# Optimization experiments

Measured on AMD Instinct MI355X. Metric: run time of the kernel, lower is better.

## Reference

```python
import jax, jax.numpy as jnp
import numpy as np

# Index conventions from the original repo's stop net
STOP_NET_STOP_IX = 0
STOP_NET_CONTINUE_IX = 1

T = 65536   # trajectory length
B = 64      # number of options (b)
A = 32      # number of low-level actions (a)


def setup_inputs() -> dict:
    key = jax.random.key(0)
    k1, k2, k3, k4 = jax.random.split(key, 4)
    # Normalized log-probabilities, as produced by abstract_policy_net
    action_logps = jax.nn.log_softmax(jax.random.normal(k1, (T + 1, B, A), jnp.float32), axis=-1)
    stop_logps = jax.nn.log_softmax(jax.random.normal(k2, (T + 1, B, 2), jnp.float32), axis=-1)
    start_logps = jax.nn.log_softmax(jax.random.normal(k3, (T + 1, B), jnp.float32), axis=-1)
    actions = jax.random.randint(k4, (T,), 0, A)
    return {
        "action_logps": action_logps,
        "stop_logps": stop_logps,
        "start_logps": start_logps,
        "actions": actions,
    }


def _hmm_neg_logp(action_logps, stop_logps, start_logps, actions):
    Tlen = actions.shape[0]
    b = start_logps.shape[1]
    # chosen-action log-probs per timestep: (T, b) = action_logps[i, :, actions[i]]
    ac = jnp.take_along_axis(action_logps[:Tlen], actions[:, None, None], axis=2)[..., 0]
    f0 = start_logps[0] + ac[0]                      # (b,)
    eye = jnp.eye(b, dtype=bool)

    def step(f_prev, xs):
        stop_i, start_i, ac_i = xs                   # (b,2), (b,), (b,)
        beta = stop_i[:, STOP_NET_STOP_IX]           # log p(stop)
        omb = stop_i[:, STOP_NET_CONTINUE_IX]        # log p(continue)
        # trans_fn[i,j] = logaddexp(beta_i + start_j, [i==j] * omb_i)
        m = beta[:, None] + start_i[None, :]         # (b, b)
        trans = jnp.where(eye, jnp.logaddexp(m, omb[:, None]), m)
        f = jax.nn.logsumexp(f_prev[:, None] + trans, axis=0) + ac_i
        return f, None

    xs = (stop_logps[1:Tlen], start_logps[1:Tlen], ac[1:Tlen])
    f, _ = jax.lax.scan(step, f0, xs)
    total_logp = jax.nn.logsumexp(f + stop_logps[Tlen, :, STOP_NET_STOP_IX])
    return -total_logp


def reference(action_logps, stop_logps, start_logps, actions):
    return _hmm_neg_logp(action_logps, stop_logps, start_logps, actions)
```

## Files before the change

kernel.cpp:

```cpp
#include <hip/hip_runtime.h>
#include <math.h>

#define T_LEN 65536
#define CHUNK 128
#define NCHUNK 512

#define CONS_BYTES ((size_t)T_LEN * 192 * 4)
#define BUFA_OFF   CONS_BYTES
#define BUFA_BYTES ((size_t)NCHUNK * 4096 * 4)
#define BUFB_OFF   (BUFA_OFF + BUFA_BYTES)
#define BUFB_BYTES ((size_t)(NCHUNK / 2) * 4096 * 4)
#define WS_NEEDED  (BUFB_OFF + BUFB_BYTES)

__global__ __launch_bounds__(256) void k_prep(const float* __restrict__ alp,
                                              const float* __restrict__ stp,
                                              const float* __restrict__ srt,
                                              const int* __restrict__ act,
                                              float* __restrict__ cons) {
    int gid = blockIdx.x * 256 + threadIdx.x;
    int t = gid >> 6;
    int b = gid & 63;
    if (t >= T_LEN) return;
    int a = act[t];
    float ac = __expf(alp[(size_t)t * 2048 + b * 32 + a]);
    float sp = __expf(srt[t * 64 + b]);
    float2 st2 = ((const float2*)stp)[t * 64 + b];
    float bp = __expf(st2.x);
    float cp = __expf(st2.y);
    size_t o = (size_t)t * 192 + b;
    cons[o]       = ac * sp;
    cons[o + 64]  = ac * cp;
    cons[o + 128] = bp;
}

#define K2_LOAD(BUF, II) do {                                                  \
    int ic_ = (II); if (ic_ > T_LEN - 1) ic_ = T_LEN - 1;                      \
    const float4* p_ = (const float4*)(cons + (size_t)ic_ * 192 + r0);         \
    const float4* q_ = (const float4*)(cons + (size_t)ic_ * 192 + 64 + r0);    \
    const float4* s_ = (const float4*)(cons + (size_t)ic_ * 192 + 128 + r0);   \
    _Pragma("unroll") for (int u = 0; u < 4; ++u) as##BUF[u] = p_[u];          \
    _Pragma("unroll") for (int u = 0; u < 4; ++u) aw##BUF[u] = q_[u];          \
    _Pragma("unroll") for (int u = 0; u < 4; ++u) bp##BUF[u] = s_[u];          \
} while (0)

#define K2_STEP(BUF, JJ) do {                                                  \
    const int i_ = ibase + (JJ);                                               \
    if (i_ < T_LEN) {                                                          \
        float sp_ = 0.f;                                                       \
        _Pragma("unroll")                                                      \
        for (int u = 0; u < 4; ++u) {                                          \
            sp_ += bp##BUF[u].x * m[4*u+0] + bp##BUF[u].y * m[4*u+1]           \
                 + bp##BUF[u].z * m[4*u+2] + bp##BUF[u].w * m[4*u+3];          \
        }                                                                      \
        part[g][col] = sp_;                                                    \
        __syncthreads();                                                       \
        float sig = part[0][col] + part[1][col] + part[2][col] + part[3][col]; \
        __syncthreads();                                                       \
        _Pragma("unroll")                                                      \
        for (int u = 0; u < 4; ++u) {                                          \
            m[4*u+0] = fmaf(aw##BUF[u].x, m[4*u+0], as##BUF[u].x * sig);       \
            m[4*u+1] = fmaf(aw##BUF[u].y, m[4*u+1], as##BUF[u].y * sig);       \
            m[4*u+2] = fmaf(aw##BUF[u].z, m[4*u+2], as##BUF[u].z * sig);       \
            m[4*u+3] = fmaf(aw##BUF[u].w, m[4*u+3], as##BUF[u].w * sig);       \
        }                                                                      \
        if (((JJ) & 3) == 3) {                                                 \
            float mxv = 0.f;                                                   \
            _Pragma("unroll")                                                  \
            for (int k = 0; k < 16; ++k) mxv = fmaxf(mxv, m[k]);               \
            part[g][col] = mxv;                                                \
            __syncthreads();                                                   \
            float cmax = fmaxf(fmaxf(part[0][col], part[1][col]),              \
                               fmaxf(part[2][col], part[3][col]));             \
            __syncthreads();                                                   \
            if (cmax > 0.f) {                                                  \
                float inv = 1.0f / cmax;                                       \
                _Pragma("unroll")                                              \
                for (int k = 0; k < 16; ++k) m[k] *= inv;                      \
                lsc += __logf(cmax);                                           \
            } else { lsc = -1e30f; }                                           \
        }                                                                      \
    }                                                                          \
} while (0)

__global__ __launch_bounds__(256) void k_chunk(const float* __restrict__ cons,
                                               float* __restrict__ mats) {
    const int tid = threadIdx.x;
    const int col = tid & 63;
    const int g = tid >> 6;
    const int r0 = __builtin_amdgcn_readfirstlane(g << 4);
    __shared__ float part[4][64];
    float m[16];
#pragma unroll
    for (int k = 0; k < 16; ++k) m[k] = (r0 + k == col) ? 1.0f : 0.0f;
    float lsc = 0.0f;
    const int chunk = blockIdx.x;
    const int ibase = 1 + chunk * CHUNK;

    float4 as0[4], aw0[4], bp0[4], as1[4], aw1[4], bp1[4];
    K2_LOAD(0, ibase);
#pragma unroll 1
    for (int j = 0; j < CHUNK; j += 2) {
        K2_LOAD(1, ibase + j + 1);
        K2_STEP(0, j);
        K2_LOAD(0, ibase + j + 2);
        K2_STEP(1, j + 1);
    }

    float* out = mats + (size_t)chunk * 4096;
#pragma unroll
    for (int k = 0; k < 16; ++k) {
        float v = (m[k] > 0.f) ? (__logf(m[k]) + lsc) : -1e30f;
        out[(r0 + k) * 64 + col] = fmaxf(v, -1e30f);
    }
}

__global__ __launch_bounds__(256) void k_combine(const float* __restrict__ in,
                                                 float* __restrict__ out) {
    __shared__ float Es[4096];
    __shared__ float Ls[4096];
    const int tid = threadIdx.x;
    const int bid = blockIdx.x;
    const float* Ein = in + (size_t)(2 * bid) * 4096;
    const float* Lin = in + (size_t)(2 * bid + 1) * 4096;
    for (int idx = tid; idx < 1024; idx += 256) {
        ((float4*)Es)[idx] = ((const float4*)Ein)[idx];
        ((float4*)Ls)[idx] = ((const float4*)Lin)[idx];
    }
    __syncthreads();
    const int col = tid & 63;
    const int r0 = (tid >> 6) << 4;
    float mx[16], sm[16];
#pragma unroll
    for (int u = 0; u < 16; ++u) { mx[u] = -3.4e38f; sm[u] = 0.f; }
#pragma unroll 1
    for (int kt = 0; kt < 4; ++kt) {
        float ec[16];
#pragma unroll
        for (int q = 0; q < 16; ++q) ec[q] = Es[(kt * 16 + q) * 64 + col];
#pragma unroll
        for (int u = 0; u < 16; ++u) {
            const float4* lr = (const float4*)(Ls + (r0 + u) * 64 + kt * 16);
#pragma unroll
            for (int q4 = 0; q4 < 4; ++q4) {
                float4 l4 = lr[q4];
                float t0 = fmaxf(l4.x + ec[4*q4+0], l4.y + ec[4*q4+1]);
                float t1 = fmaxf(l4.z + ec[4*q4+2], l4.w + ec[4*q4+3]);
                mx[u] = fmaxf(mx[u], fmaxf(t0, t1));
            }
        }
    }
#pragma unroll 1
    for (int kt = 0; kt < 4; ++kt) {
        float ec[16];
#pragma unroll
        for (int q = 0; q < 16; ++q) ec[q] = Es[(kt * 16 + q) * 64 + col];
#pragma unroll
        for (int u = 0; u < 16; ++u) {
            const float4* lr = (const float4*)(Ls + (r0 + u) * 64 + kt * 16);
#pragma unroll
            for (int q4 = 0; q4 < 4; ++q4) {
                float4 l4 = lr[q4];
                sm[u] += __expf(l4.x + ec[4*q4+0] - mx[u]);
                sm[u] += __expf(l4.y + ec[4*q4+1] - mx[u]);
                sm[u] += __expf(l4.z + ec[4*q4+2] - mx[u]);
                sm[u] += __expf(l4.w + ec[4*q4+3] - mx[u]);
            }
        }
    }
    float* o = out + (size_t)bid * 4096;
#pragma unroll
    for (int u = 0; u < 16; ++u) {
        float v = mx[u] + __logf(sm[u]);
        o[(r0 + u) * 64 + col] = fmaxf(v, -1e30f);
    }
}

__global__ __launch_bounds__(256) void k_final(const float* __restrict__ mats,
                                               const float* __restrict__ alp,
                                               const float* __restrict__ stp,
                                               const float* __restrict__ srt,
                                               const int* __restrict__ act,
                                               float* __restrict__ out) {
    __shared__ float f[64];
    __shared__ float matl[64 * 65];
    __shared__ float part[4][64];
    const int tid = threadIdx.x;
    const int r = tid & 63;
    const int g = tid >> 6;
    if (tid < 64) {
        int a0 = act[0];
        f[tid] = srt[tid] + alp[tid * 32 + a0];
    }
    __syncthreads();
#pragma unroll 1
    for (int mi = 0; mi < 32; ++mi) {
        const float* M = mats + (size_t)mi * 4096;
        for (int idx = tid; idx < 1024; idx += 256) {
            float4 v = ((const float4*)M)[idx];
            int rr = idx >> 4;
            int c0 = (idx & 15) * 4;
            matl[rr * 65 + c0 + 0] = v.x;
            matl[rr * 65 + c0 + 1] = v.y;
            matl[rr * 65 + c0 + 2] = v.z;
            matl[rr * 65 + c0 + 3] = v.w;
        }
        __syncthreads();
        float bm = -3.4e38f;
#pragma unroll
        for (int q = 0; q < 16; ++q) {
            int c = g * 16 + q;
            bm = fmaxf(bm, matl[r * 65 + c] + f[c]);
        }
        part[g][r] = bm;
        __syncthreads();
        float mxr = fmaxf(fmaxf(part[0][r], part[1][r]),
                          fmaxf(part[2][r], part[3][r]));
        __syncthreads();
        float s = 0.f;
#pragma unroll
        for (int q = 0; q < 16; ++q) {
            int c = g * 16 + q;
            s += __expf(matl[r * 65 + c] + f[c] - mxr);
        }
        part[g][r] = s;
        __syncthreads();
        if (g == 0) {
            float st = part[0][r] + part[1][r] + part[2][r] + part[3][r];
            f[r] = fmaxf(mxr + __logf(st), -1e30f);
        }
        __syncthreads();
    }
    if (tid < 64) {
        part[0][tid] = f[tid] + stp[(size_t)T_LEN * 128 + 2 * tid];
    }
    __syncthreads();
    if (tid == 0) {
        float mxx = -3.4e38f;
        for (int c = 0; c < 64; ++c) mxx = fmaxf(mxx, part[0][c]);
        float s = 0.f;
        for (int c = 0; c < 64; ++c) s += __expf(part[0][c] - mxx);
        out[0] = -(mxx + __logf(s));
    }
}

__global__ void k_wsfail(float* out, float v) { out[0] = v; }

extern "C" void kernel_launch(void* const* d_in, const int* in_sizes, int n_in,
                              void* d_out, int out_size, void* d_ws, size_t ws_size,
                              hipStream_t stream) {
    const float* alp = (const float*)d_in[0];
    const float* stp = (const float*)d_in[1];
    const float* srt = (const float*)d_in[2];
    const int* act = (const int*)d_in[3];
    float* outp = (float*)d_out;

    if (ws_size < WS_NEEDED) {
        k_wsfail<<<1, 1, 0, stream>>>(outp, (float)ws_size);
        return;
    }
    char* ws = (char*)d_ws;
    float* cons = (float*)ws;
    float* bufA = (float*)(ws + BUFA_OFF);
    float* bufB = (float*)(ws + BUFB_OFF);

    k_prep<<<dim3(16384), dim3(256), 0, stream>>>(alp, stp, srt, act, cons);
    k_chunk<<<dim3(NCHUNK), dim3(256), 0, stream>>>(cons, bufA);
    k_combine<<<dim3(256), dim3(256), 0, stream>>>(bufA, bufB);
    k_combine<<<dim3(128), dim3(256), 0, stream>>>(bufB, bufA);
    k_combine<<<dim3(64),  dim3(256), 0, stream>>>(bufA, bufB);
    k_combine<<<dim3(32),  dim3(256), 0, stream>>>(bufB, bufA);
    k_final<<<dim3(1), dim3(256), 0, stream>>>(bufA, alp, stp, srt, act, outp);
}
```

Before: 969.0 us.

## Fuse input prep into chunk scan with LDS double-buffered groups; prefetch final matrices

Removes the separate k_prep kernel and its intermediate buffer of about 50MB. The chunk kernel now gathers raw log-probs for groups of 8 steps, exponentiates them, and stages them in double-buffered shared memory while the recurrence runs on the previous group. k_final also prefetches the next matrix into registers before computing the current one. The aim is to cut global write and read traffic plus one launch, at the cost of extra shared-memory syncs and more scattered gather loads inside the latency-bound scan.

```diff
diff --git a/kernel.cpp b/kernel.cpp
--- a/kernel.cpp
+++ b/kernel.cpp
@@ -4,91 +4,27 @@
 #define T_LEN 65536
 #define CHUNK 128
 #define NCHUNK 512
-
-#define CONS_BYTES ((size_t)T_LEN * 192 * 4)
-#define BUFA_OFF   CONS_BYTES
+#define GSTEP 8
+#define NGROUP (CHUNK / GSTEP)
+
 #define BUFA_BYTES ((size_t)NCHUNK * 4096 * 4)
-#define BUFB_OFF   (BUFA_OFF + BUFA_BYTES)
 #define BUFB_BYTES ((size_t)(NCHUNK / 2) * 4096 * 4)
-#define WS_NEEDED  (BUFB_OFF + BUFB_BYTES)
-
-__global__ __launch_bounds__(256) void k_prep(const float* __restrict__ alp,
-                                              const float* __restrict__ stp,
-                                              const float* __restrict__ srt,
-                                              const int* __restrict__ act,
-                                              float* __restrict__ cons) {
-    int gid = blockIdx.x * 256 + threadIdx.x;
-    int t = gid >> 6;
-    int b = gid & 63;
-    if (t >= T_LEN) return;
-    int a = act[t];
-    float ac = __expf(alp[(size_t)t * 2048 + b * 32 + a]);
-    float sp = __expf(srt[t * 64 + b]);
-    float2 st2 = ((const float2*)stp)[t * 64 + b];
-    float bp = __expf(st2.x);
-    float cp = __expf(st2.y);
-    size_t o = (size_t)t * 192 + b;
-    cons[o]       = ac * sp;
-    cons[o + 64]  = ac * cp;
-    cons[o + 128] = bp;
-}
-
-#define K2_LOAD(BUF, II) do {                                                  \
-    int ic_ = (II); if (ic_ > T_LEN - 1) ic_ = T_LEN - 1;                      \
-    const float4* p_ = (const float4*)(cons + (size_t)ic_ * 192 + r0);         \
-    const float4* q_ = (const float4*)(cons + (size_t)ic_ * 192 + 64 + r0);    \
-    const float4* s_ = (const float4*)(cons + (size_t)ic_ * 192 + 128 + r0);   \
-    _Pragma("unroll") for (int u = 0; u < 4; ++u) as##BUF[u] = p_[u];          \
-    _Pragma("unroll") for (int u = 0; u < 4; ++u) aw##BUF[u] = q_[u];          \
-    _Pragma("unroll") for (int u = 0; u < 4; ++u) bp##BUF[u] = s_[u];          \
-} while (0)
-
-#define K2_STEP(BUF, JJ) do {                                                  \
-    const int i_ = ibase + (JJ);                                               \
-    if (i_ < T_LEN) {                                                          \
-        float sp_ = 0.f;                                                       \
-        _Pragma("unroll")                                                      \
-        for (int u = 0; u < 4; ++u) {                                          \
-            sp_ += bp##BUF[u].x * m[4*u+0] + bp##BUF[u].y * m[4*u+1]           \
-                 + bp##BUF[u].z * m[4*u+2] + bp##BUF[u].w * m[4*u+3];          \
-        }                                                                      \
-        part[g][col] = sp_;                                                    \
-        __syncthreads();                                                       \
-        float sig = part[0][col] + part[1][col] + part[2][col] + part[3][col]; \
-        __syncthreads();                                                       \
-        _Pragma("unroll")                                                      \
-        for (int u = 0; u < 4; ++u) {                                          \
-            m[4*u+0] = fmaf(aw##BUF[u].x, m[4*u+0], as##BUF[u].x * sig);       \
-            m[4*u+1] = fmaf(aw##BUF[u].y, m[4*u+1], as##BUF[u].y * sig);       \
-            m[4*u+2] = fmaf(aw##BUF[u].z, m[4*u+2], as##BUF[u].z * sig);       \
-            m[4*u+3] = fmaf(aw##BUF[u].w, m[4*u+3], as##BUF[u].w * sig);       \
-        }                                                                      \
-        if (((JJ) & 3) == 3) {                                                 \
-            float mxv = 0.f;                                                   \
-            _Pragma("unroll")                                                  \
-            for (int k = 0; k < 16; ++k) mxv = fmaxf(mxv, m[k]);               \
-            part[g][col] = mxv;                                                \
-            __syncthreads();                                                   \
-            float cmax = fmaxf(fmaxf(part[0][col], part[1][col]),              \
-                               fmaxf(part[2][col], part[3][col]));             \
-            __syncthreads();                                                   \
-            if (cmax > 0.f) {                                                  \
-                float inv = 1.0f / cmax;                                       \
-                _Pragma("unroll")                                              \
-                for (int k = 0; k < 16; ++k) m[k] *= inv;                      \
-                lsc += __logf(cmax);                                           \
-            } else { lsc = -1e30f; }                                           \
-        }                                                                      \
-    }                                                                          \
-} while (0)
-
-__global__ __launch_bounds__(256) void k_chunk(const float* __restrict__ cons,
-                                               float* __restrict__ mats) {
+#define WS_NEEDED  (BUFA_BYTES + BUFB_BYTES)
+
+__global__ __launch_bounds__(256) void k_fchunk(const float* __restrict__ alp,
+                                                const float* __restrict__ stp,
+                                                const float* __restrict__ srt,
+                                                const int* __restrict__ act,
+                                                float* __restrict__ mats) {
     const int tid = threadIdx.x;
     const int col = tid & 63;
-    const int g = tid >> 6;
-    const int r0 = __builtin_amdgcn_readfirstlane(g << 4);
+    const int wv  = tid >> 6;
+    const int r0  = wv << 4;
     __shared__ float part[4][64];
+    __shared__ float sAS[2][GSTEP][64];
+    __shared__ float sAW[2][GSTEP][64];
+    __shared__ float sBP[2][GSTEP][64];
+
     float m[16];
 #pragma unroll
     for (int k = 0; k < 16; ++k) m[k] = (r0 + k == col) ? 1.0f : 0.0f;
@@ -96,14 +32,93 @@
     const int chunk = blockIdx.x;
     const int ibase = 1 + chunk * CHUNK;
 
-    float4 as0[4], aw0[4], bp0[4], as1[4], aw1[4], bp1[4];
-    K2_LOAD(0, ibase);
-#pragma unroll 1
-    for (int j = 0; j < CHUNK; j += 2) {
-        K2_LOAD(1, ibase + j + 1);
-        K2_STEP(0, j);
-        K2_LOAD(0, ibase + j + 2);
-        K2_STEP(1, j + 1);
+    float ga[2], gs[2];
+    float2 gp[2];
+    int pad[2];
+
+    auto load_group = [&](int gg) {
+#pragma unroll
+        for (int h = 0; h < 2; ++h) {
+            int i = ibase + gg * GSTEP + wv + 4 * h;
+            pad[h] = (i >= T_LEN);
+            int ia = pad[h] ? T_LEN : i;
+            int aidx = act[pad[h] ? (T_LEN - 1) : i];
+            ga[h] = alp[(size_t)ia * 2048 + col * 32 + aidx];
+            gs[h] = srt[ia * 64 + col];
+            gp[h] = ((const float2*)stp)[ia * 64 + col];
+        }
+    };
+    auto write_group = [&](int buf) {
+#pragma unroll
+        for (int h = 0; h < 2; ++h) {
+            int s = wv + 4 * h;
+            float as_v = pad[h] ? 0.0f : __expf(ga[h] + gs[h]);
+            float aw_v = pad[h] ? 1.0f : __expf(ga[h] + gp[h].y);
+            float bp_v = pad[h] ? 0.0f : __expf(gp[h].x);
+            sAS[buf][s][col] = as_v;
+            sAW[buf][s][col] = aw_v;
+            sBP[buf][s][col] = bp_v;
+        }
+    };
+
+    load_group(0);
+    write_group(0);
+    __syncthreads();
+    int cur = 0;
+
+#pragma unroll 1
+    for (int gg = 0; gg < NGROUP; ++gg) {
+        if (gg + 1 < NGROUP) load_group(gg + 1);
+#pragma unroll
+        for (int j = 0; j < GSTEP; ++j) {
+            float4 asv[4], awv[4], bpv[4];
+            const float4* pAS = (const float4*)(&sAS[cur][j][r0]);
+            const float4* pAW = (const float4*)(&sAW[cur][j][r0]);
+            const float4* pBP = (const float4*)(&sBP[cur][j][r0]);
+#pragma unroll
+            for (int u = 0; u < 4; ++u) asv[u] = pAS[u];
+#pragma unroll
+            for (int u = 0; u < 4; ++u) awv[u] = pAW[u];
+#pragma unroll
+            for (int u = 0; u < 4; ++u) bpv[u] = pBP[u];
+            float sp_ = 0.f;
+#pragma unroll
+            for (int u = 0; u < 4; ++u) {
+                sp_ += bpv[u].x * m[4*u+0] + bpv[u].y * m[4*u+1]
+                     + bpv[u].z * m[4*u+2] + bpv[u].w * m[4*u+3];
+            }
+            part[wv][col] = sp_;
+            __syncthreads();
+            float sig = part[0][col] + part[1][col] + part[2][col] + part[3][col];
+            __syncthreads();
+#pragma unroll
+            for (int u = 0; u < 4; ++u) {
+                m[4*u+0] = fmaf(awv[u].x, m[4*u+0], asv[u].x * sig);
+                m[4*u+1] = fmaf(awv[u].y, m[4*u+1], asv[u].y * sig);
+                m[4*u+2] = fmaf(awv[u].z, m[4*u+2], asv[u].z * sig);
+                m[4*u+3] = fmaf(awv[u].w, m[4*u+3], asv[u].w * sig);
+            }
+            int jabs = gg * GSTEP + j;
+            if ((jabs & 3) == 3) {
+                float mxv = 0.f;
+#pragma unroll
+                for (int k = 0; k < 16; ++k) mxv = fmaxf(mxv, m[k]);
+                part[wv][col] = mxv;
+                __syncthreads();
+                float cmax = fmaxf(fmaxf(part[0][col], part[1][col]),
+                                   fmaxf(part[2][col], part[3][col]));
+                __syncthreads();
+                if (cmax > 0.f) {
+                    float inv = 1.0f / cmax;
+#pragma unroll
+                    for (int k = 0; k < 16; ++k) m[k] *= inv;
+                    lsc += __logf(cmax);
+                } else { lsc = -1e30f; }
+            }
+        }
+        if (gg + 1 < NGROUP) write_group(cur ^ 1);
+        __syncthreads();
+        cur ^= 1;
     }
 
     float* out = mats + (size_t)chunk * 4096;
@@ -191,20 +206,30 @@
         int a0 = act[0];
         f[tid] = srt[tid] + alp[tid * 32 + a0];
     }
-    __syncthreads();
-#pragma unroll 1
-    for (int mi = 0; mi < 32; ++mi) {
-        const float* M = mats + (size_t)mi * 4096;
-        for (int idx = tid; idx < 1024; idx += 256) {
-            float4 v = ((const float4*)M)[idx];
+    float4 pre[4];
+#pragma unroll
+    for (int u = 0; u < 4; ++u) pre[u] = ((const float4*)mats)[tid + 256 * u];
+    auto write_m = [&]() {
+#pragma unroll
+        for (int u = 0; u < 4; ++u) {
+            int idx = tid + 256 * u;
             int rr = idx >> 4;
             int c0 = (idx & 15) * 4;
-            matl[rr * 65 + c0 + 0] = v.x;
-            matl[rr * 65 + c0 + 1] = v.y;
-            matl[rr * 65 + c0 + 2] = v.z;
-            matl[rr * 65 + c0 + 3] = v.w;
-        }
-        __syncthreads();
+            matl[rr * 65 + c0 + 0] = pre[u].x;
+            matl[rr * 65 + c0 + 1] = pre[u].y;
+            matl[rr * 65 + c0 + 2] = pre[u].z;
+            matl[rr * 65 + c0 + 3] = pre[u].w;
+        }
+    };
+    write_m();
+    __syncthreads();
+#pragma unroll 1
+    for (int mi = 0; mi < 32; ++mi) {
+        if (mi + 1 < 32) {
+            const float* M = mats + (size_t)(mi + 1) * 4096;
+#pragma unroll
+            for (int u = 0; u < 4; ++u) pre[u] = ((const float4*)M)[tid + 256 * u];
+        }
         float bm = -3.4e38f;
 #pragma unroll
         for (int q = 0; q < 16; ++q) {
@@ -224,6 +249,7 @@
         }
         part[g][r] = s;
         __syncthreads();
+        if (mi + 1 < 32) write_m();
         if (g == 0) {
             float st = part[0][r] + part[1][r] + part[2][r] + part[3][r];
             f[r] = fmaxf(mxr + __logf(st), -1e30f);
@@ -259,12 +285,10 @@
         return;
     }
     char* ws = (char*)d_ws;
-    float* cons = (float*)ws;
-    float* bufA = (float*)(ws + BUFA_OFF);
-    float* bufB = (float*)(ws + BUFB_OFF);
-
-    k_prep<<<dim3(16384), dim3(256), 0, stream>>>(alp, stp, srt, act, cons);
-    k_chunk<<<dim3(NCHUNK), dim3(256), 0, stream>>>(cons, bufA);
+    float* bufA = (float*)ws;
+    float* bufB = (float*)(ws + BUFA_BYTES);
+
+    k_fchunk<<<dim3(NCHUNK), dim3(256), 0, stream>>>(alp, stp, srt, act, bufA);
     k_combine<<<dim3(256), dim3(256), 0, stream>>>(bufA, bufB);
     k_combine<<<dim3(128), dim3(256), 0, stream>>>(bufB, bufA);
     k_combine<<<dim3(64),  dim3(256), 0, stream>>>(bufA, bufB);
```

New measurement: 815.6 us. -15.8%, faster.
